# Optimization experiments

Measured on AMD Instinct MI355X. Metric: run time of the kernel, lower is better.

## Reference

```python
import jax, jax.numpy as jnp
import numpy as np

MATRIX_DIM = 128
FEAT = MATRIX_DIM * (MATRIX_DIM + 1) // 2  # 8256, triu incl. diagonal
HID = FEAT // 5                            # 1651
BATCH = 4096


def setup_inputs() -> dict:
    key = jax.random.key(0)
    k0, k1, k2, k3, k4 = jax.random.split(key, 5)
    stdv1 = 1.0 / FEAT / 2.0
    stdv2 = 1.0 / HID / 2.0
    return {
        "sim_matrices": jax.random.normal(k0, (BATCH, MATRIX_DIM, MATRIX_DIM), dtype=jnp.float32),
        "W1": jax.random.uniform(k1, (HID, FEAT), minval=-stdv1, maxval=stdv1, dtype=jnp.float32),
        "b1": jax.random.uniform(k2, (HID,), minval=-stdv1, maxval=stdv1, dtype=jnp.float32),
        "W2": jax.random.uniform(k3, (1, HID), minval=-stdv2, maxval=stdv2, dtype=jnp.float32),
        "b2": jax.random.uniform(k4, (1,), minval=-stdv2, maxval=stdv2, dtype=jnp.float32),
    }


def reference(sim_matrices, W1, b1, W2, b2):
    # flatten: take upper-triangular (incl. diag) entries -> [B, FEAT]
    iu0, iu1 = np.triu_indices(sim_matrices.shape[1])
    x = sim_matrices[:, iu0, iu1]
    # Linear_block 1 (ideal crossbar VMM = W x + b) + ReLU
    h = jax.nn.relu(jnp.einsum("bf,hf->bh", x, W1) + b1)
    # Linear_block 2 + Sigmoid -> [B, 1]
    return jax.nn.sigmoid(jnp.einsum("bh,oh->bo", h, W2) + b2)
```

## Files before the change

kernel.cpp:

```cpp
#include <hip/hip_runtime.h>
#include <hip/hip_bf16.h>
#include <math.h>

#define MDIM  128
#define FEAT  8256
#define HID   1651
#define HIDP  1664
#define BATCH 4096
#define BK    64
#define KT_TOTAL 129
#define NZ    2
#define KT_PER 64
#define W1SCALE 8192.0f
#define W1INV   (1.0f / 8192.0f)

using f32x4  = __attribute__((ext_vector_type(4))) float;
using f32x16 = __attribute__((ext_vector_type(16))) float;
using i32x4  = __attribute__((ext_vector_type(4))) int;
using i32x8  = __attribute__((ext_vector_type(8))) int;
using bf16x8 = __attribute__((ext_vector_type(8))) __bf16;
typedef long long i64;

__device__ __forceinline__ void gload_lds16(const void* g, void* l) {
    __builtin_amdgcn_global_load_lds(
        (const __attribute__((address_space(1))) void*)g,
        (__attribute__((address_space(3))) void*)l,
        16, 0, 0);
}

__device__ __forceinline__ int row_off(int i) { return (i * (257 - i)) >> 1; }

__device__ __forceinline__ void pack8_fp8(const float* f, int* o) {
    int lo = __builtin_amdgcn_cvt_pk_fp8_f32(f[0], f[1], 0, false);
    lo     = __builtin_amdgcn_cvt_pk_fp8_f32(f[2], f[3], lo, true);
    int hi = __builtin_amdgcn_cvt_pk_fp8_f32(f[4], f[5], 0, false);
    hi     = __builtin_amdgcn_cvt_pk_fp8_f32(f[6], f[7], hi, true);
    o[0] = lo; o[1] = hi;
}

__global__ void __launch_bounds__(256)
prep_kernel(const float* __restrict__ sim, const float* __restrict__ W1,
            char* __restrict__ X, char* __restrict__ W1p) {
    const int t = threadIdx.x;
    if (blockIdx.x < BATCH) {
        const int b = blockIdx.x;
        const float* srow = sim + ((i64)b << 14);
        char* dst = X + (i64)b * FEAT;
#pragma unroll
        for (int it = 0; it < 5; ++it) {
            const int w = it * 256 + t;
            if (w < FEAT / 8) {
                const int f0 = w * 8;
                int i = (int)((257.0f - sqrtf(66049.0f - 8.0f * (float)f0)) * 0.5f);
                i = i < 0 ? 0 : (i > 127 ? 127 : i);
                while (i < 127 && row_off(i + 1) <= f0) ++i;
                while (i > 0 && row_off(i) > f0) --i;
                int j = i + (f0 - row_off(i));
                float v[8];
#pragma unroll
                for (int e = 0; e < 8; ++e) {
                    if (j > 127) { ++i; j = i; }
                    v[e] = srow[i * MDIM + j];
                    ++j;
                }
                int o[2];
                pack8_fp8(v, o);
                *(int2*)(dst + f0) = make_int2(o[0], o[1]);
            }
        }
    } else {
        const int c  = blockIdx.x - BATCH;
        const int wb = c % 5;
        const int n  = c / 5;
        const int w  = wb * 256 + t;
        if (w >= FEAT / 8) return;
        const int f0 = w * 8;
        int o[2];
        if (n < HID) {
            const float* src = W1 + (i64)n * FEAT + f0;
            const f32x4 a = *(const f32x4*)src;
            const f32x4 d = *(const f32x4*)(src + 4);
            float v[8];
#pragma unroll
            for (int e = 0; e < 4; ++e) {
                v[e]     = a[e] * W1SCALE;
                v[e + 4] = d[e] * W1SCALE;
            }
            pack8_fp8(v, o);
        } else {
            o[0] = 0; o[1] = 0;
        }
        *(int2*)(W1p + (i64)n * FEAT + f0) = make_int2(o[0], o[1]);
    }
}

__global__ void __launch_bounds__(256, 4)
gemm_split_kernel(const char* __restrict__ X,
                  const char* __restrict__ W1p,
                  __hip_bfloat16* __restrict__ Cz) {
    __shared__ __align__(16) char lds_a[2 * 8192];
    __shared__ __align__(16) char lds_b[2 * 8192];

    const int t    = threadIdx.x;
    const int w    = t >> 6;
    const int l    = t & 63;
    const int bm   = blockIdx.x;
    const int bn   = blockIdx.y;
    const int z    = blockIdx.z;
    const int wm   = w >> 1;
    const int wn   = w & 1;
    const int lm   = l & 31;
    const int c0   = (l >> 5) << 1;

    f32x16 acc[2][2];
#pragma unroll
    for (int r = 0; r < 16; ++r) {
        acc[0][0][r] = 0.f; acc[0][1][r] = 0.f;
        acc[1][0][r] = 0.f; acc[1][1][r] = 0.f;
    }

    const int kt0 = z * KT_PER;
    const int nkt = (z == NZ - 1) ? (KT_TOTAL - KT_PER * (NZ - 1)) : KT_PER;

    const int stR = ((w & 1) << 6) + l;
    const int stC = w >> 1;
    const char* gA0 = X + (i64)(bm * 128 + stR) * FEAT + kt0 * BK + stC * 16;
    const char* gB0 = W1p + (i64)(bn * 128 + stR) * FEAT + kt0 * BK + stC * 16;
    char* lA = lds_a + w * 1024;
    char* lB = lds_b + w * 1024;

#define STAGE(bufoff, kidx) do {                                   \
        const char* _ga = gA0 + (i64)(kidx) * BK;                  \
        const char* _gb = gB0 + (i64)(kidx) * BK;                  \
        gload_lds16(_ga,      lA + (bufoff));                      \
        gload_lds16(_ga + 32, lA + (bufoff) + 4096);               \
        gload_lds16(_gb,      lB + (bufoff));                      \
        gload_lds16(_gb + 32, lB + (bufoff) + 4096);               \
    } while (0)

    STAGE(0, 0);
    __syncthreads();

    int cur = 0;
    for (int kt = 0; kt < nkt; ++kt) {
        const int nxt = cur ^ 1;
        if (kt + 1 < nkt) STAGE(nxt * 8192, kt + 1);

        const char* pa = lds_a + cur * 8192 + c0 * 2048 + (wm * 64 + lm) * 16;
        const char* pb = lds_b + cur * 8192 + c0 * 2048 + (wn * 64 + lm) * 16;
        const i32x4 a0l = *(const i32x4*)(pa);
        const i32x4 a0h = *(const i32x4*)(pa + 2048);
        const i32x4 a1l = *(const i32x4*)(pa + 512);
        const i32x4 a1h = *(const i32x4*)(pa + 512 + 2048);
        const i32x4 b0l = *(const i32x4*)(pb);
        const i32x4 b0h = *(const i32x4*)(pb + 2048);
        const i32x4 b1l = *(const i32x4*)(pb + 512);
        const i32x4 b1h = *(const i32x4*)(pb + 512 + 2048);
        const i32x8 A0 = __builtin_shufflevector(a0l, a0h, 0, 1, 2, 3, 4, 5, 6, 7);
        const i32x8 A1 = __builtin_shufflevector(a1l, a1h, 0, 1, 2, 3, 4, 5, 6, 7);
        const i32x8 B0 = __builtin_shufflevector(b0l, b0h, 0, 1, 2, 3, 4, 5, 6, 7);
        const i32x8 B1 = __builtin_shufflevector(b1l, b1h, 0, 1, 2, 3, 4, 5, 6, 7);

        acc[0][0] = __builtin_amdgcn_mfma_scale_f32_32x32x64_f8f6f4(
            A0, B0, acc[0][0], 0, 0, 0, 0x7F7F7F7F, 0, 0x7F7F7F7F);
        acc[0][1] = __builtin_amdgcn_mfma_scale_f32_32x32x64_f8f6f4(
            A0, B1, acc[0][1], 0, 0, 0, 0x7F7F7F7F, 0, 0x7F7F7F7F);
        acc[1][0] = __builtin_amdgcn_mfma_scale_f32_32x32x64_f8f6f4(
            A1, B0, acc[1][0], 0, 0, 0, 0x7F7F7F7F, 0, 0x7F7F7F7F);
        acc[1][1] = __builtin_amdgcn_mfma_scale_f32_32x32x64_f8f6f4(
            A1, B1, acc[1][1], 0, 0, 0, 0x7F7F7F7F, 0, 0x7F7F7F7F);

        __syncthreads();
        cur = nxt;
    }
#undef STAGE

    __hip_bfloat16* cz = Cz + ((i64)z * BATCH + bm * 128) * HIDP
                            + bn * 128 + wn * 64;
#pragma unroll
    for (int rb = 0; rb < 2; ++rb)
#pragma unroll
        for (int cb = 0; cb < 2; ++cb) {
#pragma unroll
            for (int reg = 0; reg < 16; ++reg) {
                const int row = (reg & 3) + ((reg >> 2) << 3) + ((l >> 5) << 2);
                const int ml  = wm * 64 + rb * 32 + row;
                cz[(i64)ml * HIDP + cb * 32 + lm] =
                    __float2bfloat16(acc[rb][cb][reg]);
            }
        }
}

__global__ void __launch_bounds__(256)
epilogue_kernel(const __hip_bfloat16* __restrict__ Cz,
                const float* __restrict__ b1,
                const float* __restrict__ W2,
                const float* __restrict__ b2,
                float* __restrict__ out) {
    const int b = blockIdx.x;
    const int t = threadIdx.x;
    float sum = 0.0f;
    const bf16x8* r0 = (const bf16x8*)(Cz + (i64)b * HIDP);
    const bf16x8* r1 = (const bf16x8*)(Cz + ((i64)BATCH + b) * HIDP);
    if (t < HIDP / 8) {
        const bf16x8 a = r0[t];
        const bf16x8 c = r1[t];
#pragma unroll
        for (int e = 0; e < 8; ++e) {
            const int n = t * 8 + e;
            if (n < HID) {
                const float v = ((float)a[e] + (float)c[e]) * W1INV + b1[n];
                sum += fmaxf(v, 0.0f) * W2[n];
            }
        }
    }
    sum += __shfl_xor(sum, 1);
    sum += __shfl_xor(sum, 2);
    sum += __shfl_xor(sum, 4);
    sum += __shfl_xor(sum, 8);
    sum += __shfl_xor(sum, 16);
    sum += __shfl_xor(sum, 32);
    __shared__ float wsum[4];
    if ((t & 63) == 0) wsum[t >> 6] = sum;
    __syncthreads();
    if (t == 0) {
        const float s = wsum[0] + wsum[1] + wsum[2] + wsum[3];
        out[b] = 1.0f / (1.0f + expf(-(s + b2[0])));
    }
}

extern "C" void kernel_launch(void* const* d_in, const int* in_sizes, int n_in,
                              void* d_out, int out_size, void* d_ws, size_t ws_size,
                              hipStream_t stream) {
    const float* sim = (const float*)d_in[0];
    const float* W1  = (const float*)d_in[1];
    const float* b1  = (const float*)d_in[2];
    const float* W2  = (const float*)d_in[3];
    const float* b2  = (const float*)d_in[4];
    float* out = (float*)d_out;

    char* ws = (char*)d_ws;
    const i64 X_OFF   = 0;
    const i64 W1P_OFF = (i64)BATCH * FEAT;
    const i64 CZ_OFF  = W1P_OFF + (i64)HIDP * FEAT;
    char*           Xf8  = ws + X_OFF;
    char*           W1f8 = ws + W1P_OFF;
    __hip_bfloat16* Cz   = (__hip_bfloat16*)(ws + CZ_OFF);

    prep_kernel<<<BATCH + 5 * HIDP, 256, 0, stream>>>(sim, W1, Xf8, W1f8);
    {
        dim3 grid(BATCH / 128, HIDP / 128, NZ);
        gemm_split_kernel<<<grid, 256, 0, stream>>>(Xf8, W1f8, Cz);
    }
    epilogue_kernel<<<BATCH, 256, 0, stream>>>(Cz, b1, W2, b2, out);
}
```

Measured before the change: 525.8 us.

## Deepen GEMM LDS pipeline to three stages with explicit vmcnt waits

Replaces double-buffered LDS staging with a three-deep ring buffer, prefetching three k-tiles ahead and waiting with explicit s_waitcnt vmcnt counts instead of a full __syncthreads drain. It also raises wave priority around the MFMA block and inserts sched_barriers to keep the ordering fixed. The aim is to hide global-to-LDS latency better. In exchange LDS use grows to 48KB per block and launch bounds drop to 3 blocks/CU, so occupancy may fall. The hand-counted vmcnt values are also fragile if the compiler emits other vector memory ops.

Result: no change. 527.4 us (+0.3%).

```diff
diff --git a/kernel.cpp b/kernel.cpp
--- a/kernel.cpp
+++ b/kernel.cpp
@@ -13,6 +13,7 @@
 #define KT_PER 64
 #define W1SCALE 8192.0f
 #define W1INV   (1.0f / 8192.0f)
+#define DEPTH 3
 
 using f32x4  = __attribute__((ext_vector_type(4))) float;
 using f32x16 = __attribute__((ext_vector_type(16))) float;
@@ -94,12 +95,12 @@
     }
 }
 
-__global__ void __launch_bounds__(256, 4)
+__global__ void __launch_bounds__(256, 3)
 gemm_split_kernel(const char* __restrict__ X,
                   const char* __restrict__ W1p,
                   __hip_bfloat16* __restrict__ Cz) {
-    __shared__ __align__(16) char lds_a[2 * 8192];
-    __shared__ __align__(16) char lds_b[2 * 8192];
+    __shared__ __align__(16) char lds_a[DEPTH * 8192];
+    __shared__ __align__(16) char lds_b[DEPTH * 8192];
 
     const int t    = threadIdx.x;
     const int w    = t >> 6;
@@ -123,44 +124,47 @@
     const int nkt = (z == NZ - 1) ? (KT_TOTAL - KT_PER * (NZ - 1)) : KT_PER;
 
     const int stR = ((w & 1) << 6) + l;
-    const int stC = w >> 1;
-    const char* gA0 = X + (i64)(bm * 128 + stR) * FEAT + kt0 * BK + stC * 16;
-    const char* gB0 = W1p + (i64)(bn * 128 + stR) * FEAT + kt0 * BK + stC * 16;
+    const char* gA0 = X + (i64)(bm * 128 + stR) * FEAT + kt0 * BK + (w >> 1) * 16;
+    const char* gB0 = W1p + (i64)(bn * 128 + stR) * FEAT + kt0 * BK + (w >> 1) * 16;
     char* lA = lds_a + w * 1024;
     char* lB = lds_b + w * 1024;
 
-#define STAGE(bufoff, kidx) do {                                   \
+#define STAGE(buf, kidx) do {                                      \
         const char* _ga = gA0 + (i64)(kidx) * BK;                  \
         const char* _gb = gB0 + (i64)(kidx) * BK;                  \
-        gload_lds16(_ga,      lA + (bufoff));                      \
-        gload_lds16(_ga + 32, lA + (bufoff) + 4096);               \
-        gload_lds16(_gb,      lB + (bufoff));                      \
-        gload_lds16(_gb + 32, lB + (bufoff) + 4096);               \
+        char* _la = lA + (buf) * 8192;                             \
+        char* _lb = lB + (buf) * 8192;                             \
+        gload_lds16(_ga,      _la);                                \
+        gload_lds16(_ga + 32, _la + 4096);                         \
+        gload_lds16(_gb,      _lb);                                \
+        gload_lds16(_gb + 32, _lb + 4096);                         \
     } while (0)
 
     STAGE(0, 0);
-    __syncthreads();
+    STAGE(1, 1);
+    STAGE(2, 2);
 
     int cur = 0;
     for (int kt = 0; kt < nkt; ++kt) {
-        const int nxt = cur ^ 1;
-        if (kt + 1 < nkt) STAGE(nxt * 8192, kt + 1);
+        if (kt + 3 <= nkt)      asm volatile("s_waitcnt vmcnt(8)" ::: "memory");
+        else if (kt + 2 == nkt) asm volatile("s_waitcnt vmcnt(4)" ::: "memory");
+        else                    asm volatile("s_waitcnt vmcnt(0)" ::: "memory");
+        __builtin_amdgcn_s_barrier();
+        __builtin_amdgcn_sched_barrier(0);
 
         const char* pa = lds_a + cur * 8192 + c0 * 2048 + (wm * 64 + lm) * 16;
         const char* pb = lds_b + cur * 8192 + c0 * 2048 + (wn * 64 + lm) * 16;
-        const i32x4 a0l = *(const i32x4*)(pa);
-        const i32x4 a0h = *(const i32x4*)(pa + 2048);
-        const i32x4 a1l = *(const i32x4*)(pa + 512);
-        const i32x4 a1h = *(const i32x4*)(pa + 512 + 2048);
-        const i32x4 b0l = *(const i32x4*)(pb);
-        const i32x4 b0h = *(const i32x4*)(pb + 2048);
-        const i32x4 b1l = *(const i32x4*)(pb + 512);
-        const i32x4 b1h = *(const i32x4*)(pb + 512 + 2048);
-        const i32x8 A0 = __builtin_shufflevector(a0l, a0h, 0, 1, 2, 3, 4, 5, 6, 7);
-        const i32x8 A1 = __builtin_shufflevector(a1l, a1h, 0, 1, 2, 3, 4, 5, 6, 7);
-        const i32x8 B0 = __builtin_shufflevector(b0l, b0h, 0, 1, 2, 3, 4, 5, 6, 7);
-        const i32x8 B1 = __builtin_shufflevector(b1l, b1h, 0, 1, 2, 3, 4, 5, 6, 7);
-
+        i32x8 A0, A1, B0, B1;
+        *((i32x4*)&A0)     = *(const i32x4*)(pa);
+        *((i32x4*)&A0 + 1) = *(const i32x4*)(pa + 2048);
+        *((i32x4*)&A1)     = *(const i32x4*)(pa + 512);
+        *((i32x4*)&A1 + 1) = *(const i32x4*)(pa + 512 + 2048);
+        *((i32x4*)&B0)     = *(const i32x4*)(pb);
+        *((i32x4*)&B0 + 1) = *(const i32x4*)(pb + 2048);
+        *((i32x4*)&B1)     = *(const i32x4*)(pb + 512);
+        *((i32x4*)&B1 + 1) = *(const i32x4*)(pb + 512 + 2048);
+
+        __builtin_amdgcn_s_setprio(1);
         acc[0][0] = __builtin_amdgcn_mfma_scale_f32_32x32x64_f8f6f4(
             A0, B0, acc[0][0], 0, 0, 0, 0x7F7F7F7F, 0, 0x7F7F7F7F);
         acc[0][1] = __builtin_amdgcn_mfma_scale_f32_32x32x64_f8f6f4(
@@ -169,9 +173,15 @@
             A1, B0, acc[1][0], 0, 0, 0, 0x7F7F7F7F, 0, 0x7F7F7F7F);
         acc[1][1] = __builtin_amdgcn_mfma_scale_f32_32x32x64_f8f6f4(
             A1, B1, acc[1][1], 0, 0, 0, 0x7F7F7F7F, 0, 0x7F7F7F7F);
-
-        __syncthreads();
-        cur = nxt;
+        __builtin_amdgcn_s_setprio(0);
+
+        asm volatile("s_waitcnt lgkmcnt(0)" ::: "memory");
+        __builtin_amdgcn_sched_barrier(0);
+        __builtin_amdgcn_s_barrier();
+        __builtin_amdgcn_sched_barrier(0);
+
+        if (kt + 3 < nkt) STAGE(cur, kt + 3);
+        cur = (cur == DEPTH - 1) ? 0 : cur + 1;
     }
 #undef STAGE
 
```
